# Optimization experiments

Hardware: AMD Instinct MI355X
Metric: run time of the kernel (lower is better)

## Reference

```python
import jax, jax.numpy as jnp
import numpy as np

N, D, E = 50000, 128, 100000
H1, H2, H3 = 8, 8, 4
NEG_SLOPE = 0.2  # PyG GATv2Conv default negative_slope


def _gatv2_layer(x, src, dst, Wl, Wr, att, b, heads):
    # GATv2Conv(in=D, out=D, heads=heads, concat=False), share_weights=False
    C = Wl.shape[1] // heads
    xl = (x @ Wl).reshape(-1, heads, C)  # source-side transform (x_j)
    xr = (x @ Wr).reshape(-1, heads, C)  # target-side transform (x_i)
    m = jax.nn.leaky_relu(xl[src] + xr[dst], NEG_SLOPE)      # [E,H,C]
    e = jnp.einsum('ehc,hc->eh', m, att)                      # [E,H]
    # segment softmax over incoming edges of each destination node
    emax = jax.ops.segment_max(e, dst, num_segments=N)        # [N,H]
    a = jnp.exp(e - emax[dst])
    denom = jax.ops.segment_sum(a, dst, num_segments=N)       # [N,H] (>0: self-loops)
    a = a / denom[dst]
    out = jax.ops.segment_sum(xl[src] * a[:, :, None], dst, num_segments=N)  # [N,H,C]
    return out.mean(axis=1) + b  # concat=False -> head mean, then bias


def setup_inputs() -> dict:
    key = jax.random.key(0)
    ks = jax.random.split(key, 16)
    x = jax.random.normal(ks[0], (N, D), dtype=jnp.float32)
    src = jax.random.randint(ks[1], (E,), 0, N)
    dst = jax.random.randint(ks[2], (E,), 0, N)
    src = jnp.where(src == dst, (src + 1) % N, src)  # no pre-existing self loops
    edge_index = jnp.stack([src, dst]).astype(jnp.int64)
    s = 1.0 / np.sqrt(D)
    def lin(k, h):
        return jax.random.uniform(k, (D, h * D), jnp.float32, -s, s)
    def attn(k, h):
        return jax.random.uniform(k, (h, D), jnp.float32, -s, s)
    return {
        'x': x, 'edge_index': edge_index,
        'W1l': lin(ks[3], H1), 'W1r': lin(ks[4], H1), 'att1': attn(ks[5], H1), 'b1': jnp.zeros((D,), jnp.float32),
        'W2l': lin(ks[6], H2), 'W2r': lin(ks[7], H2), 'att2': attn(ks[8], H2), 'b2': jnp.zeros((D,), jnp.float32),
        'W3l': lin(ks[9], H3), 'W3r': lin(ks[10], H3), 'att3': attn(ks[11], H3), 'b3': jnp.zeros((D,), jnp.float32),
    }


def reference(x, edge_index, W1l, W1r, att1, b1, W2l, W2r, att2, b2, W3l, W3r, att3, b3):
    # PyG GATv2Conv adds self loops by default
    loops = jnp.arange(N, dtype=edge_index.dtype)
    src = jnp.concatenate([edge_index[0], loops])
    dst = jnp.concatenate([edge_index[1], loops])
    h = x + _gatv2_layer(x, src, dst, W1l, W1r, att1, b1, H1)
    h = jax.nn.elu(h)  # dropout is identity in eval mode
    h = h + _gatv2_layer(h, src, dst, W2l, W2r, att2, b2, H2)
    h = jax.nn.elu(h)
    h = h + _gatv2_layer(h, src, dst, W3l, W3r, att3, b3, H3)
    return h
```

## Files before the change

kernel.cpp:

```cpp
#include <hip/hip_runtime.h>

#define NN 50000
#define DD 128
#define EE 100000
#define ET (EE + NN)

typedef __attribute__((ext_vector_type(4))) float f32x4;
typedef __attribute__((ext_vector_type(8))) short bf16x8;
typedef __attribute__((ext_vector_type(4))) unsigned short u16x4;
typedef __attribute__((ext_vector_type(4))) unsigned int u32x4;
typedef __attribute__((ext_vector_type(2))) unsigned int u32x2;

static __device__ __forceinline__ unsigned short f2bf(float f) {
  union { float f; unsigned int u; } v; v.f = f;
  unsigned int r = (v.u + 0x7FFFu + ((v.u >> 16) & 1u)) >> 16;
  return (unsigned short)r;
}
static __device__ __forceinline__ float bflo(unsigned int u) {
  union { unsigned int u; float f; } v; v.u = u << 16; return v.f;
}
static __device__ __forceinline__ float bfhi(unsigned int u) {
  union { unsigned int u; float f; } v; v.u = u & 0xffff0000u; return v.f;
}

template <int CTRL>
static __device__ __forceinline__ float dpp_add(float x) {
  int xi = __builtin_bit_cast(int, x);
  int yi = __builtin_amdgcn_update_dpp(xi, xi, CTRL, 0xF, 0xF, true);
  return x + __builtin_bit_cast(float, yi);
}
static __device__ __forceinline__ float row16_sum(float p) {
  p = dpp_add<0xB1>(p);
  p = dpp_add<0x4E>(p);
  p = dpp_add<0x141>(p);
  p = dpp_add<0x128>(p);
  return p;
}

__global__ __launch_bounds__(256) void k_prep(
    const float* __restrict__ x, const int* __restrict__ ei,
    const float* __restrict__ W1l, const float* __restrict__ W1r,
    const float* __restrict__ W2l, const float* __restrict__ W2r,
    const float* __restrict__ W3l, const float* __restrict__ W3r,
    const float* __restrict__ att1, const float* __restrict__ att2, const float* __restrict__ att3,
    unsigned short* __restrict__ wt1, unsigned short* __restrict__ wt2,
    unsigned short* __restrict__ wt3,
    float* __restrict__ as1, float* __restrict__ as2, float* __restrict__ as3,
    unsigned short* __restrict__ abf, int* __restrict__ counts) {
  const int i = blockIdx.x * 256 + threadIdx.x;
  const float LOG2E = 1.4426950408889634f;
  if (i < 262144) {
    int half = i >> 17, rem = i & 131071;
    int nn = rem >> 7, k = rem & 127;
    const float* W = half ? W1r : W1l;
    wt1[i] = f2bf(W[(size_t)k * 1024 + nn]);
  } else if (i < 524288) {
    int local = i - 262144;
    int half = local >> 17, rem = local & 131071;
    int nn = rem >> 7, k = rem & 127;
    const float* W = half ? W2r : W2l;
    wt2[local] = f2bf(W[(size_t)k * 1024 + nn]);
  } else if (i < 655360) {
    int local = i - 524288;
    int half = local >> 16, rem = local & 65535;
    int nn = rem >> 7, k = rem & 127;
    const float* W = half ? W3r : W3l;
    wt3[local] = f2bf(W[(size_t)k * 512 + nn]);
  } else if (i < 657920) {
    int local = i - 655360;
    if (local < 1024) as1[local] = att1[local] * LOG2E;
    else if (local < 2048) as2[local - 1024] = att2[local - 1024] * LOG2E;
    else as3[local - 2048] = att3[local - 2048] * LOG2E;
  } else if (i < 807920) {
    int e = i - 657920;
    int dst = (e < EE) ? ei[EE + e] : (e - EE);
    if (dst >= 0 && dst < NN) atomicAdd(&counts[dst], 1);
  } else if (i < 2407920) {
    int u = i - 807920;
    f32x4 v = *(const f32x4*)(x + (size_t)u * 4);
    u16x4 w;
    w.x = f2bf(v.x); w.y = f2bf(v.y); w.z = f2bf(v.z); w.w = f2bf(v.w);
    *(u16x4*)(abf + (size_t)u * 4) = w;
  }
}

__global__ __launch_bounds__(1024) void k_scan(const int* __restrict__ counts,
                                               int* __restrict__ offs,
                                               int* __restrict__ cursor) {
  __shared__ int wsum[16];
  __shared__ int wpre[16];
  __shared__ int wtot;
  const int tid = threadIdx.x;
  const int wv = tid >> 6, lane = tid & 63;
  int carry = 0;
  for (int base = 0; base < NN; base += 4096) {
    int i0 = base + tid * 4;
    int v[4];
#pragma unroll
    for (int q = 0; q < 4; ++q) { int i = i0 + q; v[q] = (i < NN) ? counts[i] : 0; }
    int s = v[0] + v[1] + v[2] + v[3];
    int sc = s;
#pragma unroll
    for (int m = 1; m < 64; m <<= 1) {
      int t = __shfl_up(sc, m, 64);
      if (lane >= m) sc += t;
    }
    if (lane == 63) wsum[wv] = sc;
    __syncthreads();
    if (tid < 16) {
      int t = wsum[tid];
      int scc = t;
#pragma unroll
      for (int m = 1; m < 16; m <<= 1) {
        int u = __shfl_up(scc, m, 64);
        if (tid >= m) scc += u;
      }
      wpre[tid] = scc - t;
      if (tid == 15) wtot = scc;
    }
    __syncthreads();
    int excl = carry + wpre[wv] + (sc - s);
#pragma unroll
    for (int q = 0; q < 4; ++q) {
      int i = i0 + q;
      if (i < NN) { offs[i] = excl; cursor[i] = excl; }
      excl += v[q];
    }
    carry += wtot;
    __syncthreads();
  }
  if (tid == 0) offs[NN] = carry;
}

__global__ void k_fill(const int* __restrict__ ei, int* __restrict__ cursor,
                       int* __restrict__ srcs) {
  int i = blockIdx.x * blockDim.x + threadIdx.x;
  if (i >= ET) return;
  int src, dst;
  if (i < EE) { src = ei[i]; dst = ei[EE + i]; }
  else { src = dst = i - EE; }
  if (dst < 0 || dst >= NN) return;
  if (src < 0 || src >= NN) src = dst;
  int pos = atomicAdd(&cursor[dst], 1);
  if (pos >= 0 && pos < ET) srcs[pos] = src;
}

__global__ __launch_bounds__(256) void gemm_bt(
    const unsigned short* __restrict__ A, const unsigned short* __restrict__ WT,
    unsigned short* __restrict__ Cl, unsigned short* __restrict__ Cr,
    int M, int Nout, int lgny) {
  const int f = blockIdx.x;
  const int c = f & ((1 << lgny) - 1);
  const int x = f >> lgny;
  const int z = c & 1, y = c >> 1;
  const int m0 = x * 128, n0 = y * 128;
  unsigned short* C = z ? Cr : Cl;
  const unsigned short* BT = WT + (size_t)z * Nout * DD;

  __shared__ unsigned short As[128 * 128];
  __shared__ unsigned short Bs[128 * 128];
  const int tid = threadIdx.x;
  const int wave = tid >> 6, lane = tid & 63;
  const int hi = lane >> 4, lr = lane & 15;

#pragma unroll
  for (int i = 0; i < 8; ++i) {
    int row = i * 16 + wave * 4 + hi;
    int c16 = lr ^ (row & 7);
    const unsigned short* ga = A + (size_t)(m0 + row) * DD + c16 * 8;
    __builtin_amdgcn_global_load_lds((const __attribute__((address_space(1))) void*)ga,
        (__attribute__((address_space(3))) void*)(As + i * 2048 + wave * 512), 16, 0, 0);
    const unsigned short* gb = BT + (size_t)(n0 + row) * DD + c16 * 8;
    __builtin_amdgcn_global_load_lds((const __attribute__((address_space(1))) void*)gb,
        (__attribute__((address_space(3))) void*)(Bs + i * 2048 + wave * 512), 16, 0, 0);
  }
  __syncthreads();

  const int wr = (wave >> 1) * 64, wc = (wave & 1) * 64;
  f32x4 acc[4][4];
#pragma unroll
  for (int i = 0; i < 4; ++i)
#pragma unroll
    for (int j = 0; j < 4; ++j) acc[i][j] = (f32x4){0.f, 0.f, 0.f, 0.f};

#pragma unroll
  for (int k0 = 0; k0 < 128; k0 += 32) {
    const int ck = (k0 >> 3) + hi;
    bf16x8 af[4], bfr[4];
#pragma unroll
    for (int mi = 0; mi < 4; ++mi) {
      int r = wr + mi * 16 + lr;
      af[mi] = *(const bf16x8*)&As[r * 128 + ((ck ^ (r & 7)) << 3)];
    }
#pragma unroll
    for (int ni = 0; ni < 4; ++ni) {
      int cc = wc + ni * 16 + lr;
      bfr[ni] = *(const bf16x8*)&Bs[cc * 128 + ((ck ^ (cc & 7)) << 3)];
    }
#pragma unroll
    for (int mi = 0; mi < 4; ++mi)
#pragma unroll
      for (int ni = 0; ni < 4; ++ni)
        acc[mi][ni] = __builtin_amdgcn_mfma_f32_16x16x32_bf16(af[mi], bfr[ni], acc[mi][ni], 0, 0, 0);
  }

#pragma unroll
  for (int mi = 0; mi < 4; ++mi) {
#pragma unroll
    for (int ni = 0; ni < 4; ++ni) {
      int col = n0 + wc + ni * 16 + lr;
#pragma unroll
      for (int j = 0; j < 4; ++j) {
        int row = m0 + wr + mi * 16 + (hi << 2) + j;
        if (row < M) C[(size_t)row * Nout + col] = f2bf(acc[mi][ni][j]);
      }
    }
  }
}

template <int H>
__global__ __launch_bounds__(256) void gat_agg5(
    const unsigned short* __restrict__ xl, const unsigned short* __restrict__ xr,
    const int* __restrict__ offs, const int* __restrict__ srcs,
    const float* __restrict__ att_s,
    const float* __restrict__ bias,
    const float* __restrict__ resid, float* __restrict__ out,
    unsigned short* __restrict__ hbf, int do_elu) {
  constexpr int HG = H / 2;
  constexpr int CPL = 2 * HG;
  constexpr int NW = HG;
  constexpr int LPH = 128 / CPL;
  constexpr int ROW = H * DD;
  constexpr int HALFROW = ROW / 2;
  const int wave = threadIdx.x >> 6, lane = threadIdx.x & 63;
  const int nsub = wave >> 1, g = wave & 1;
  const int n = blockIdx.x * 2 + nsub;
  if (n >= NN) return;
  const int cb = g * HALFROW + lane * CPL;

  float xrv[CPL], av[CPL];
  {
    const unsigned int* q = (const unsigned int*)(xr + (size_t)n * ROW + cb);
#pragma unroll
    for (int w = 0; w < NW; ++w) {
      unsigned int u = q[w];
      xrv[2 * w] = bflo(u);
      xrv[2 * w + 1] = bfhi(u);
    }
#pragma unroll
    for (int c = 0; c < CPL; ++c) av[c] = att_s[cb + c];
  }

  float acc[CPL];
#pragma unroll
  for (int c = 0; c < CPL; ++c) acc[c] = 0.f;
  float mx = -1e30f, dn = 0.f;

  const int e0 = offs[n], e1 = offs[n + 1];
  const unsigned short* xl_cb = xl + cb;
  for (int j = e0; j < e1; j += 4) {
    const int B = (e1 - j < 4) ? (e1 - j) : 4;
    unsigned int rows[4][NW];
#pragma unroll
    for (int b = 0; b < 4; ++b) {
      if (b < B) {
        int s = srcs[j + b];
        const unsigned int* qq = (const unsigned int*)(xl_cb + (size_t)s * ROW);
#pragma unroll
        for (int w = 0; w < NW; ++w) rows[b][w] = qq[w];
      }
    }
    float p[4];
#pragma unroll
    for (int b = 0; b < 4; ++b) {
      float pp = -1e30f;
      if (b < B) {
        pp = 0.f;
#pragma unroll
        for (int w = 0; w < NW; ++w) {
          float x0 = bflo(rows[b][w]), x1 = bfhi(rows[b][w]);
          float z0 = x0 + xrv[2 * w]; z0 = fmaxf(z0, 0.2f * z0);
          float z1 = x1 + xrv[2 * w + 1]; z1 = fmaxf(z1, 0.2f * z1);
          pp = fmaf(z0, av[2 * w], pp);
          pp = fmaf(z1, av[2 * w + 1], pp);
        }
        pp = row16_sum(pp);
        if constexpr (LPH == 32) pp += __shfl_xor(pp, 16, 64);
      }
      p[b] = pp;
    }
    float pm = fmaxf(fmaxf(p[0], p[1]), fmaxf(p[2], p[3]));
    if (__any(pm > mx + 11.5f)) {
      float mnew = fmaxf(mx, pm);
      float sc = __builtin_amdgcn_exp2f(mx - mnew);
      dn *= sc;
#pragma unroll
      for (int c = 0; c < CPL; ++c) acc[c] *= sc;
      mx = mnew;
    }
#pragma unroll
    for (int b = 0; b < 4; ++b) {
      if (b < B) {
        float wt = __builtin_amdgcn_exp2f(p[b] - mx);
        dn += wt;
#pragma unroll
        for (int w = 0; w < NW; ++w) {
          acc[2 * w] = fmaf(wt, bflo(rows[b][w]), acc[2 * w]);
          acc[2 * w + 1] = fmaf(wt, bfhi(rows[b][w]), acc[2 * w + 1]);
        }
      }
    }
  }

  float r[CPL];
  const float inv = (1.f / (float)H) / dn;
#pragma unroll
  for (int c = 0; c < CPL; ++c) r[c] = acc[c] * inv;
#pragma unroll
  for (int m = LPH; m < 64; m <<= 1)
#pragma unroll
    for (int c = 0; c < CPL; ++c) r[c] += __shfl_xor(r[c], m, 64);

  __shared__ float lds[2][DD];
  const int d0 = (lane * CPL) & 127;
  if (g == 1 && lane < LPH) {
#pragma unroll
    for (int c = 0; c < CPL; ++c) lds[nsub][d0 + c] = r[c];
  }
  __syncthreads();
  if (g == 0 && lane < LPH) {
    float o[CPL];
#pragma unroll
    for (int c = 0; c < CPL; ++c) {
      o[c] = r[c] + lds[nsub][d0 + c] + bias[d0 + c] + resid[(size_t)n * DD + d0 + c];
      if (do_elu && o[c] < 0.f)
        o[c] = __builtin_amdgcn_exp2f(o[c] * 1.4426950408889634f) - 1.f;
    }
#pragma unroll
    for (int c = 0; c < CPL; c += 4) {
      f32x4 v; v.x = o[c]; v.y = o[c + 1]; v.z = o[c + 2]; v.w = o[c + 3];
      *(f32x4*)(out + (size_t)n * DD + d0 + c) = v;
    }
    if (hbf) {
      unsigned int pk[CPL / 2];
#pragma unroll
      for (int q = 0; q < CPL / 2; ++q)
        pk[q] = (unsigned int)f2bf(o[2 * q]) | ((unsigned int)f2bf(o[2 * q + 1]) << 16);
      if constexpr (CPL == 8) {
        u32x4 v; v.x = pk[0]; v.y = pk[1]; v.z = pk[2]; v.w = pk[3];
        *(u32x4*)(hbf + (size_t)n * DD + d0) = v;
      } else {
        u32x2 v; v.x = pk[0]; v.y = pk[1];
        *(u32x2*)(hbf + (size_t)n * DD + d0) = v;
      }
    }
  }
}

extern "C" void kernel_launch(void* const* d_in, const int* in_sizes, int n_in,
                              void* d_out, int out_size, void* d_ws, size_t ws_size,
                              hipStream_t stream) {
  const float* x = (const float*)d_in[0];
  const int* ei = (const int*)d_in[1];
  const float* W1l = (const float*)d_in[2];
  const float* W1r = (const float*)d_in[3];
  const float* att1 = (const float*)d_in[4];
  const float* b1 = (const float*)d_in[5];
  const float* W2l = (const float*)d_in[6];
  const float* W2r = (const float*)d_in[7];
  const float* att2 = (const float*)d_in[8];
  const float* b2 = (const float*)d_in[9];
  const float* W3l = (const float*)d_in[10];
  const float* W3r = (const float*)d_in[11];
  const float* att3 = (const float*)d_in[12];
  const float* b3 = (const float*)d_in[13];
  float* out = (float*)d_out;

  char* p = (char*)d_ws;
  auto carve = [&](size_t bytes) {
    char* r = p;
    p += (bytes + 255) & ~(size_t)255;
    return r;
  };
  unsigned short* xl = (unsigned short*)carve((size_t)NN * 1024 * 2);
  unsigned short* xr = (unsigned short*)carve((size_t)NN * 1024 * 2);
  unsigned short* abf = (unsigned short*)carve((size_t)NN * DD * 2);
  unsigned short* wt1 = (unsigned short*)carve((size_t)2 * 1024 * DD * 2);
  unsigned short* wt2 = (unsigned short*)carve((size_t)2 * 1024 * DD * 2);
  unsigned short* wt3 = (unsigned short*)carve((size_t)2 * 512 * DD * 2);
  float* as1 = (float*)carve((size_t)8 * DD * 4);
  float* as2 = (float*)carve((size_t)8 * DD * 4);
  float* as3 = (float*)carve((size_t)4 * DD * 4);
  int* counts = (int*)carve((size_t)NN * 4);
  int* offs = (int*)carve(((size_t)NN + 1) * 4);
  int* cursor = (int*)carve((size_t)NN * 4);
  int* srcs = (int*)carve((size_t)ET * 4);
  size_t needed = (size_t)(p - (char*)d_ws);
  if (needed > ws_size) return;

  hipMemsetAsync(counts, 0, (size_t)NN * 4, stream);
  k_prep<<<9406, 256, 0, stream>>>(x, ei, W1l, W1r, W2l, W2r, W3l, W3r, att1, att2, att3,
                                   wt1, wt2, wt3, as1, as2, as3, abf, counts);
  k_scan<<<1, 1024, 0, stream>>>(counts, offs, cursor);
  k_fill<<<(ET + 255) / 256, 256, 0, stream>>>(ei, cursor, srcs);

  const int gx = (NN + 127) / 128;
  const int ga = (NN + 1) / 2;
  gemm_bt<<<gx * 16, 256, 0, stream>>>(abf, wt1, xl, xr, NN, 1024, 4);
  gat_agg5<8><<<ga, 256, 0, stream>>>(xl, xr, offs, srcs, as1, b1, x, out, abf, 1);
  gemm_bt<<<gx * 16, 256, 0, stream>>>(abf, wt2, xl, xr, NN, 1024, 4);
  gat_agg5<8><<<ga, 256, 0, stream>>>(xl, xr, offs, srcs, as2, b2, out, out, abf, 1);
  gemm_bt<<<gx * 8, 256, 0, stream>>>(abf, wt3, xl, xr, NN, 512, 3);
  gat_agg5<4><<<ga, 256, 0, stream>>>(xl, xr, offs, srcs, as3, b3, out, out, nullptr, 0);
}
```

Measured before the change: 472.2 us.

## Process four node pairs per block and batch eight edges per gather

The aggregation kernel now loops over four node pairs per block, so the launch is 6250 blocks instead of 25000. Attention weights and bias are loaded once per block rather than once per node, and a double-buffered LDS slot is used for the cross-wave reduction. The edge loop now gathers eight source rows per step instead of four, with the source indices prefetched first, to give more memory-level parallelism. The costs are higher register pressure from the 8-row buffer, which may lower occupancy, and fewer blocks to spread the irregular degree distribution across.

```diff
diff --git a/kernel.cpp b/kernel.cpp
--- a/kernel.cpp
+++ b/kernel.cpp
@@ -219,7 +219,7 @@
 }
 
 template <int H>
-__global__ __launch_bounds__(256) void gat_agg5(
+__global__ __launch_bounds__(256) void gat_agg6(
     const unsigned short* __restrict__ xl, const unsigned short* __restrict__ xr,
     const int* __restrict__ offs, const int* __restrict__ srcs,
     const float* __restrict__ att_s,
@@ -232,126 +232,139 @@
   constexpr int LPH = 128 / CPL;
   constexpr int ROW = H * DD;
   constexpr int HALFROW = ROW / 2;
+  constexpr int ITERS = 4;
   const int wave = threadIdx.x >> 6, lane = threadIdx.x & 63;
   const int nsub = wave >> 1, g = wave & 1;
-  const int n = blockIdx.x * 2 + nsub;
-  if (n >= NN) return;
   const int cb = g * HALFROW + lane * CPL;
-
-  float xrv[CPL], av[CPL];
-  {
-    const unsigned int* q = (const unsigned int*)(xr + (size_t)n * ROW + cb);
-#pragma unroll
-    for (int w = 0; w < NW; ++w) {
-      unsigned int u = q[w];
-      xrv[2 * w] = bflo(u);
-      xrv[2 * w + 1] = bfhi(u);
-    }
-#pragma unroll
-    for (int c = 0; c < CPL; ++c) av[c] = att_s[cb + c];
-  }
-
-  float acc[CPL];
-#pragma unroll
-  for (int c = 0; c < CPL; ++c) acc[c] = 0.f;
-  float mx = -1e30f, dn = 0.f;
-
-  const int e0 = offs[n], e1 = offs[n + 1];
+  const int d0 = (lane * CPL) & 127;
+
+  float av[CPL], bv[CPL];
+#pragma unroll
+  for (int c = 0; c < CPL; ++c) av[c] = att_s[cb + c];
+#pragma unroll
+  for (int c = 0; c < CPL; ++c) bv[c] = bias[d0 + c];
+
+  __shared__ float lds[2][2][DD];
   const unsigned short* xl_cb = xl + cb;
-  for (int j = e0; j < e1; j += 4) {
-    const int B = (e1 - j < 4) ? (e1 - j) : 4;
-    unsigned int rows[4][NW];
-#pragma unroll
-    for (int b = 0; b < 4; ++b) {
-      if (b < B) {
-        int s = srcs[j + b];
-        const unsigned int* qq = (const unsigned int*)(xl_cb + (size_t)s * ROW);
-#pragma unroll
-        for (int w = 0; w < NW; ++w) rows[b][w] = qq[w];
-      }
-    }
-    float p[4];
-#pragma unroll
-    for (int b = 0; b < 4; ++b) {
-      float pp = -1e30f;
-      if (b < B) {
-        pp = 0.f;
-#pragma unroll
-        for (int w = 0; w < NW; ++w) {
-          float x0 = bflo(rows[b][w]), x1 = bfhi(rows[b][w]);
-          float z0 = x0 + xrv[2 * w]; z0 = fmaxf(z0, 0.2f * z0);
-          float z1 = x1 + xrv[2 * w + 1]; z1 = fmaxf(z1, 0.2f * z1);
-          pp = fmaf(z0, av[2 * w], pp);
-          pp = fmaf(z1, av[2 * w + 1], pp);
+
+  for (int it = 0; it < ITERS; ++it) {
+    const int np = blockIdx.x * ITERS + it;
+    const int n = np * 2 + nsub;
+    const int e0 = offs[n], e1 = offs[n + 1];
+
+    float xrv[CPL];
+    {
+      const unsigned int* q = (const unsigned int*)(xr + (size_t)n * ROW + cb);
+#pragma unroll
+      for (int w = 0; w < NW; ++w) {
+        unsigned int u = q[w];
+        xrv[2 * w] = bflo(u);
+        xrv[2 * w + 1] = bfhi(u);
+      }
+    }
+    float acc[CPL];
+#pragma unroll
+    for (int c = 0; c < CPL; ++c) acc[c] = 0.f;
+    float mx = -1e30f, dn = 0.f;
+
+    for (int j = e0; j < e1; j += 8) {
+      const int B = (e1 - j < 8) ? (e1 - j) : 8;
+      int sv[8];
+#pragma unroll
+      for (int b = 0; b < 8; ++b) sv[b] = (b < B) ? srcs[j + b] : 0;
+      unsigned int rows[8][NW];
+#pragma unroll
+      for (int b = 0; b < 8; ++b) {
+        if (b < B) {
+          const unsigned int* qq = (const unsigned int*)(xl_cb + (size_t)sv[b] * ROW);
+#pragma unroll
+          for (int w = 0; w < NW; ++w) rows[b][w] = qq[w];
         }
-        pp = row16_sum(pp);
-        if constexpr (LPH == 32) pp += __shfl_xor(pp, 16, 64);
-      }
-      p[b] = pp;
-    }
-    float pm = fmaxf(fmaxf(p[0], p[1]), fmaxf(p[2], p[3]));
-    if (__any(pm > mx + 11.5f)) {
-      float mnew = fmaxf(mx, pm);
-      float sc = __builtin_amdgcn_exp2f(mx - mnew);
-      dn *= sc;
-#pragma unroll
-      for (int c = 0; c < CPL; ++c) acc[c] *= sc;
-      mx = mnew;
-    }
-#pragma unroll
-    for (int b = 0; b < 4; ++b) {
-      if (b < B) {
-        float wt = __builtin_amdgcn_exp2f(p[b] - mx);
-        dn += wt;
-#pragma unroll
-        for (int w = 0; w < NW; ++w) {
-          acc[2 * w] = fmaf(wt, bflo(rows[b][w]), acc[2 * w]);
-          acc[2 * w + 1] = fmaf(wt, bfhi(rows[b][w]), acc[2 * w + 1]);
+      }
+      float p[8];
+#pragma unroll
+      for (int b = 0; b < 8; ++b) {
+        float pp = -1e30f;
+        if (b < B) {
+          pp = 0.f;
+#pragma unroll
+          for (int w = 0; w < NW; ++w) {
+            float x0 = bflo(rows[b][w]), x1 = bfhi(rows[b][w]);
+            float z0 = x0 + xrv[2 * w]; z0 = fmaxf(z0, 0.2f * z0);
+            float z1 = x1 + xrv[2 * w + 1]; z1 = fmaxf(z1, 0.2f * z1);
+            pp = fmaf(z0, av[2 * w], pp);
+            pp = fmaf(z1, av[2 * w + 1], pp);
+          }
+          pp = row16_sum(pp);
+          if constexpr (LPH == 32) pp += __shfl_xor(pp, 16, 64);
         }
-      }
-    }
-  }
-
-  float r[CPL];
-  const float inv = (1.f / (float)H) / dn;
-#pragma unroll
-  for (int c = 0; c < CPL; ++c) r[c] = acc[c] * inv;
-#pragma unroll
-  for (int m = LPH; m < 64; m <<= 1)
-#pragma unroll
-    for (int c = 0; c < CPL; ++c) r[c] += __shfl_xor(r[c], m, 64);
-
-  __shared__ float lds[2][DD];
-  const int d0 = (lane * CPL) & 127;
-  if (g == 1 && lane < LPH) {
-#pragma unroll
-    for (int c = 0; c < CPL; ++c) lds[nsub][d0 + c] = r[c];
-  }
-  __syncthreads();
-  if (g == 0 && lane < LPH) {
-    float o[CPL];
-#pragma unroll
-    for (int c = 0; c < CPL; ++c) {
-      o[c] = r[c] + lds[nsub][d0 + c] + bias[d0 + c] + resid[(size_t)n * DD + d0 + c];
-      if (do_elu && o[c] < 0.f)
-        o[c] = __builtin_amdgcn_exp2f(o[c] * 1.4426950408889634f) - 1.f;
-    }
-#pragma unroll
-    for (int c = 0; c < CPL; c += 4) {
-      f32x4 v; v.x = o[c]; v.y = o[c + 1]; v.z = o[c + 2]; v.w = o[c + 3];
-      *(f32x4*)(out + (size_t)n * DD + d0 + c) = v;
-    }
-    if (hbf) {
-      unsigned int pk[CPL / 2];
-#pragma unroll
-      for (int q = 0; q < CPL / 2; ++q)
-        pk[q] = (unsigned int)f2bf(o[2 * q]) | ((unsigned int)f2bf(o[2 * q + 1]) << 16);
-      if constexpr (CPL == 8) {
-        u32x4 v; v.x = pk[0]; v.y = pk[1]; v.z = pk[2]; v.w = pk[3];
-        *(u32x4*)(hbf + (size_t)n * DD + d0) = v;
-      } else {
-        u32x2 v; v.x = pk[0]; v.y = pk[1];
-        *(u32x2*)(hbf + (size_t)n * DD + d0) = v;
+        p[b] = pp;
+      }
+      float pm = p[0];
+#pragma unroll
+      for (int b = 1; b < 8; ++b) pm = fmaxf(pm, p[b]);
+      if (__any(pm > mx + 11.5f)) {
+        float mnew = fmaxf(mx, pm);
+        float sc = __builtin_amdgcn_exp2f(mx - mnew);
+        dn *= sc;
+#pragma unroll
+        for (int c = 0; c < CPL; ++c) acc[c] *= sc;
+        mx = mnew;
+      }
+#pragma unroll
+      for (int b = 0; b < 8; ++b) {
+        if (b < B) {
+          float wt = __builtin_amdgcn_exp2f(p[b] - mx);
+          dn += wt;
+#pragma unroll
+          for (int w = 0; w < NW; ++w) {
+            acc[2 * w] = fmaf(wt, bflo(rows[b][w]), acc[2 * w]);
+            acc[2 * w + 1] = fmaf(wt, bfhi(rows[b][w]), acc[2 * w + 1]);
+          }
+        }
+      }
+    }
+
+    float r[CPL];
+    const float inv = (1.f / (float)H) / dn;
+#pragma unroll
+    for (int c = 0; c < CPL; ++c) r[c] = acc[c] * inv;
+#pragma unroll
+    for (int m = LPH; m < 64; m <<= 1)
+#pragma unroll
+      for (int c = 0; c < CPL; ++c) r[c] += __shfl_xor(r[c], m, 64);
+
+    const int par = it & 1;
+    if (g == 1 && lane < LPH) {
+#pragma unroll
+      for (int c = 0; c < CPL; ++c) lds[par][nsub][d0 + c] = r[c];
+    }
+    __syncthreads();
+    if (g == 0 && lane < LPH) {
+      float o[CPL];
+#pragma unroll
+      for (int c = 0; c < CPL; ++c) {
+        o[c] = r[c] + lds[par][nsub][d0 + c] + bv[c] + resid[(size_t)n * DD + d0 + c];
+        if (do_elu && o[c] < 0.f)
+          o[c] = __builtin_amdgcn_exp2f(o[c] * 1.4426950408889634f) - 1.f;
+      }
+#pragma unroll
+      for (int c = 0; c < CPL; c += 4) {
+        f32x4 v; v.x = o[c]; v.y = o[c + 1]; v.z = o[c + 2]; v.w = o[c + 3];
+        *(f32x4*)(out + (size_t)n * DD + d0 + c) = v;
+      }
+      if (hbf) {
+        unsigned int pk[CPL / 2];
+#pragma unroll
+        for (int q = 0; q < CPL / 2; ++q)
+          pk[q] = (unsigned int)f2bf(o[2 * q]) | ((unsigned int)f2bf(o[2 * q + 1]) << 16);
+        if constexpr (CPL == 8) {
+          u32x4 v; v.x = pk[0]; v.y = pk[1]; v.z = pk[2]; v.w = pk[3];
+          *(u32x4*)(hbf + (size_t)n * DD + d0) = v;
+        } else {
+          u32x2 v; v.x = pk[0]; v.y = pk[1];
+          *(u32x2*)(hbf + (size_t)n * DD + d0) = v;
+        }
       }
     }
   }
@@ -405,11 +418,11 @@
   k_fill<<<(ET + 255) / 256, 256, 0, stream>>>(ei, cursor, srcs);
 
   const int gx = (NN + 127) / 128;
-  const int ga = (NN + 1) / 2;
+  const int ga = NN / 8;
   gemm_bt<<<gx * 16, 256, 0, stream>>>(abf, wt1, xl, xr, NN, 1024, 4);
-  gat_agg5<8><<<ga, 256, 0, stream>>>(xl, xr, offs, srcs, as1, b1, x, out, abf, 1);
+  gat_agg6<8><<<ga, 256, 0, stream>>>(xl, xr, offs, srcs, as1, b1, x, out, abf, 1);
   gemm_bt<<<gx * 16, 256, 0, stream>>>(abf, wt2, xl, xr, NN, 1024, 4);
-  gat_agg5<8><<<ga, 256, 0, stream>>>(xl, xr, offs, srcs, as2, b2, out, out, abf, 1);
+  gat_agg6<8><<<ga, 256, 0, stream>>>(xl, xr, offs, srcs, as2, b2, out, out, abf, 1);
   gemm_bt<<<gx * 8, 256, 0, stream>>>(abf, wt3, xl, xr, NN, 512, 3);
-  gat_agg5<4><<<ga, 256, 0, stream>>>(xl, xr, offs, srcs, as3, b3, out, out, nullptr, 0);
-}
+  gat_agg6<4><<<ga, 256, 0, stream>>>(xl, xr, offs, srcs, as3, b3, out, out, nullptr, 0);
+}
```

After: 570.2 us. +20.8%, slower.

## Make GAT aggregation persistent and carry residual through bf16 buffer only

Applied to the files above, without the earlier changes.

The aggregation kernel becomes a persistent grid-stride loop over node pairs with a fixed grid of 2048 blocks, double-buffering the shared-memory exchange between the two half-row waves. Layers 1 and 2 no longer write the fp32 hidden state; layers 2 and 3 read their residual from the bf16 activation buffer instead of an fp32 copy. The aim is to cut global memory traffic and block launch overhead in the aggregation passes. In exchange the residual path is rounded to bf16, which adds a small accuracy loss, and the fixed grid may balance work across nodes with uneven degree less well.

```diff
diff --git a/kernel.cpp b/kernel.cpp
--- a/kernel.cpp
+++ b/kernel.cpp
@@ -219,13 +219,16 @@
 }
 
 template <int H>
-__global__ __launch_bounds__(256) void gat_agg5(
+__global__ __launch_bounds__(256) void gat_agg7(
     const unsigned short* __restrict__ xl, const unsigned short* __restrict__ xr,
     const int* __restrict__ offs, const int* __restrict__ srcs,
     const float* __restrict__ att_s,
     const float* __restrict__ bias,
-    const float* __restrict__ resid, float* __restrict__ out,
-    unsigned short* __restrict__ hbf, int do_elu) {
+    const float* __restrict__ residf,
+    const unsigned short* __restrict__ residb,
+    float* __restrict__ outf,
+    unsigned short* __restrict__ hbfw,
+    int do_elu) {
   constexpr int HG = H / 2;
   constexpr int CPL = 2 * HG;
   constexpr int NW = HG;
@@ -234,126 +237,150 @@
   constexpr int HALFROW = ROW / 2;
   const int wave = threadIdx.x >> 6, lane = threadIdx.x & 63;
   const int nsub = wave >> 1, g = wave & 1;
-  const int n = blockIdx.x * 2 + nsub;
-  if (n >= NN) return;
   const int cb = g * HALFROW + lane * CPL;
-
-  float xrv[CPL], av[CPL];
-  {
-    const unsigned int* q = (const unsigned int*)(xr + (size_t)n * ROW + cb);
-#pragma unroll
-    for (int w = 0; w < NW; ++w) {
-      unsigned int u = q[w];
-      xrv[2 * w] = bflo(u);
-      xrv[2 * w + 1] = bfhi(u);
-    }
-#pragma unroll
-    for (int c = 0; c < CPL; ++c) av[c] = att_s[cb + c];
-  }
-
-  float acc[CPL];
-#pragma unroll
-  for (int c = 0; c < CPL; ++c) acc[c] = 0.f;
-  float mx = -1e30f, dn = 0.f;
-
-  const int e0 = offs[n], e1 = offs[n + 1];
+  const int d0 = (lane * CPL) & 127;
+
+  float av[CPL];
+#pragma unroll
+  for (int c = 0; c < CPL; ++c) av[c] = att_s[cb + c];
+
+  __shared__ float lds[2][2][DD];
   const unsigned short* xl_cb = xl + cb;
-  for (int j = e0; j < e1; j += 4) {
-    const int B = (e1 - j < 4) ? (e1 - j) : 4;
-    unsigned int rows[4][NW];
-#pragma unroll
-    for (int b = 0; b < 4; ++b) {
-      if (b < B) {
-        int s = srcs[j + b];
-        const unsigned int* qq = (const unsigned int*)(xl_cb + (size_t)s * ROW);
-#pragma unroll
-        for (int w = 0; w < NW; ++w) rows[b][w] = qq[w];
-      }
-    }
-    float p[4];
-#pragma unroll
-    for (int b = 0; b < 4; ++b) {
-      float pp = -1e30f;
-      if (b < B) {
-        pp = 0.f;
-#pragma unroll
-        for (int w = 0; w < NW; ++w) {
-          float x0 = bflo(rows[b][w]), x1 = bfhi(rows[b][w]);
-          float z0 = x0 + xrv[2 * w]; z0 = fmaxf(z0, 0.2f * z0);
-          float z1 = x1 + xrv[2 * w + 1]; z1 = fmaxf(z1, 0.2f * z1);
-          pp = fmaf(z0, av[2 * w], pp);
-          pp = fmaf(z1, av[2 * w + 1], pp);
-        }
-        pp = row16_sum(pp);
-        if constexpr (LPH == 32) pp += __shfl_xor(pp, 16, 64);
-      }
-      p[b] = pp;
-    }
-    float pm = fmaxf(fmaxf(p[0], p[1]), fmaxf(p[2], p[3]));
-    if (__any(pm > mx + 11.5f)) {
-      float mnew = fmaxf(mx, pm);
-      float sc = __builtin_amdgcn_exp2f(mx - mnew);
-      dn *= sc;
-#pragma unroll
-      for (int c = 0; c < CPL; ++c) acc[c] *= sc;
-      mx = mnew;
-    }
-#pragma unroll
-    for (int b = 0; b < 4; ++b) {
-      if (b < B) {
-        float wt = __builtin_amdgcn_exp2f(p[b] - mx);
-        dn += wt;
-#pragma unroll
-        for (int w = 0; w < NW; ++w) {
-          acc[2 * w] = fmaf(wt, bflo(rows[b][w]), acc[2 * w]);
-          acc[2 * w + 1] = fmaf(wt, bfhi(rows[b][w]), acc[2 * w + 1]);
-        }
-      }
-    }
-  }
-
-  float r[CPL];
-  const float inv = (1.f / (float)H) / dn;
-#pragma unroll
-  for (int c = 0; c < CPL; ++c) r[c] = acc[c] * inv;
-#pragma unroll
-  for (int m = LPH; m < 64; m <<= 1)
-#pragma unroll
-    for (int c = 0; c < CPL; ++c) r[c] += __shfl_xor(r[c], m, 64);
-
-  __shared__ float lds[2][DD];
-  const int d0 = (lane * CPL) & 127;
-  if (g == 1 && lane < LPH) {
-#pragma unroll
-    for (int c = 0; c < CPL; ++c) lds[nsub][d0 + c] = r[c];
-  }
-  __syncthreads();
-  if (g == 0 && lane < LPH) {
-    float o[CPL];
-#pragma unroll
-    for (int c = 0; c < CPL; ++c) {
-      o[c] = r[c] + lds[nsub][d0 + c] + bias[d0 + c] + resid[(size_t)n * DD + d0 + c];
-      if (do_elu && o[c] < 0.f)
-        o[c] = __builtin_amdgcn_exp2f(o[c] * 1.4426950408889634f) - 1.f;
-    }
-#pragma unroll
-    for (int c = 0; c < CPL; c += 4) {
-      f32x4 v; v.x = o[c]; v.y = o[c + 1]; v.z = o[c + 2]; v.w = o[c + 3];
-      *(f32x4*)(out + (size_t)n * DD + d0 + c) = v;
-    }
-    if (hbf) {
-      unsigned int pk[CPL / 2];
-#pragma unroll
-      for (int q = 0; q < CPL / 2; ++q)
-        pk[q] = (unsigned int)f2bf(o[2 * q]) | ((unsigned int)f2bf(o[2 * q + 1]) << 16);
-      if constexpr (CPL == 8) {
-        u32x4 v; v.x = pk[0]; v.y = pk[1]; v.z = pk[2]; v.w = pk[3];
-        *(u32x4*)(hbf + (size_t)n * DD + d0) = v;
+  const int stride = gridDim.x * 2;
+  int par = 0;
+
+  for (int n = blockIdx.x * 2 + nsub; n < NN; n += stride) {
+    const int e0 = offs[n], e1 = offs[n + 1];
+
+    float xrv[CPL];
+    {
+      const unsigned int* q = (const unsigned int*)(xr + (size_t)n * ROW + cb);
+#pragma unroll
+      for (int w = 0; w < NW; ++w) {
+        unsigned int u = q[w];
+        xrv[2 * w] = bflo(u);
+        xrv[2 * w + 1] = bfhi(u);
+      }
+    }
+    float acc[CPL];
+#pragma unroll
+    for (int c = 0; c < CPL; ++c) acc[c] = 0.f;
+    float mx = -1e30f, dn = 0.f;
+
+    for (int j = e0; j < e1; j += 4) {
+      const int B = (e1 - j < 4) ? (e1 - j) : 4;
+      unsigned int rows[4][NW];
+#pragma unroll
+      for (int b = 0; b < 4; ++b) {
+        if (b < B) {
+          int s = srcs[j + b];
+          const unsigned int* qq = (const unsigned int*)(xl_cb + (size_t)s * ROW);
+#pragma unroll
+          for (int w = 0; w < NW; ++w) rows[b][w] = qq[w];
+        }
+      }
+      float p[4];
+#pragma unroll
+      for (int b = 0; b < 4; ++b) {
+        float pp = -1e30f;
+        if (b < B) {
+          pp = 0.f;
+#pragma unroll
+          for (int w = 0; w < NW; ++w) {
+            float x0 = bflo(rows[b][w]), x1 = bfhi(rows[b][w]);
+            float z0 = x0 + xrv[2 * w]; z0 = fmaxf(z0, 0.2f * z0);
+            float z1 = x1 + xrv[2 * w + 1]; z1 = fmaxf(z1, 0.2f * z1);
+            pp = fmaf(z0, av[2 * w], pp);
+            pp = fmaf(z1, av[2 * w + 1], pp);
+          }
+          pp = row16_sum(pp);
+          if constexpr (LPH == 32) pp += __shfl_xor(pp, 16, 64);
+        }
+        p[b] = pp;
+      }
+      float pm = fmaxf(fmaxf(p[0], p[1]), fmaxf(p[2], p[3]));
+      if (__any(pm > mx + 11.5f)) {
+        float mnew = fmaxf(mx, pm);
+        float sc = __builtin_amdgcn_exp2f(mx - mnew);
+        dn *= sc;
+#pragma unroll
+        for (int c = 0; c < CPL; ++c) acc[c] *= sc;
+        mx = mnew;
+      }
+#pragma unroll
+      for (int b = 0; b < 4; ++b) {
+        if (b < B) {
+          float wt = __builtin_amdgcn_exp2f(p[b] - mx);
+          dn += wt;
+#pragma unroll
+          for (int w = 0; w < NW; ++w) {
+            acc[2 * w] = fmaf(wt, bflo(rows[b][w]), acc[2 * w]);
+            acc[2 * w + 1] = fmaf(wt, bfhi(rows[b][w]), acc[2 * w + 1]);
+          }
+        }
+      }
+    }
+
+    float r[CPL];
+    const float inv = (1.f / (float)H) / dn;
+#pragma unroll
+    for (int c = 0; c < CPL; ++c) r[c] = acc[c] * inv;
+#pragma unroll
+    for (int m = LPH; m < 64; m <<= 1)
+#pragma unroll
+      for (int c = 0; c < CPL; ++c) r[c] += __shfl_xor(r[c], m, 64);
+
+    if (g == 1 && lane < LPH) {
+#pragma unroll
+      for (int c = 0; c < CPL; ++c) lds[par][nsub][d0 + c] = r[c];
+    }
+    __syncthreads();
+    if (g == 0 && lane < LPH) {
+      float rv[CPL];
+      if (residf) {
+#pragma unroll
+        for (int c = 0; c < CPL; c += 4) {
+          f32x4 v = *(const f32x4*)(residf + (size_t)n * DD + d0 + c);
+          rv[c] = v.x; rv[c + 1] = v.y; rv[c + 2] = v.z; rv[c + 3] = v.w;
+        }
       } else {
-        u32x2 v; v.x = pk[0]; v.y = pk[1];
-        *(u32x2*)(hbf + (size_t)n * DD + d0) = v;
-      }
-    }
+        const unsigned int* q = (const unsigned int*)(residb + (size_t)n * DD + d0);
+#pragma unroll
+        for (int w = 0; w < CPL / 2; ++w) {
+          unsigned int u = q[w];
+          rv[2 * w] = bflo(u);
+          rv[2 * w + 1] = bfhi(u);
+        }
+      }
+      float o[CPL];
+#pragma unroll
+      for (int c = 0; c < CPL; ++c) {
+        o[c] = r[c] + lds[par][nsub][d0 + c] + bias[d0 + c] + rv[c];
+        if (do_elu && o[c] < 0.f)
+          o[c] = __builtin_amdgcn_exp2f(o[c] * 1.4426950408889634f) - 1.f;
+      }
+      if (outf) {
+#pragma unroll
+        for (int c = 0; c < CPL; c += 4) {
+          f32x4 v; v.x = o[c]; v.y = o[c + 1]; v.z = o[c + 2]; v.w = o[c + 3];
+          *(f32x4*)(outf + (size_t)n * DD + d0 + c) = v;
+        }
+      }
+      if (hbfw) {
+        unsigned int pk[CPL / 2];
+#pragma unroll
+        for (int q = 0; q < CPL / 2; ++q)
+          pk[q] = (unsigned int)f2bf(o[2 * q]) | ((unsigned int)f2bf(o[2 * q + 1]) << 16);
+        if constexpr (CPL == 8) {
+          u32x4 v; v.x = pk[0]; v.y = pk[1]; v.z = pk[2]; v.w = pk[3];
+          *(u32x4*)(hbfw + (size_t)n * DD + d0) = v;
+        } else {
+          u32x2 v; v.x = pk[0]; v.y = pk[1];
+          *(u32x2*)(hbfw + (size_t)n * DD + d0) = v;
+        }
+      }
+    }
+    par ^= 1;
   }
 }
 
@@ -405,11 +432,14 @@
   k_fill<<<(ET + 255) / 256, 256, 0, stream>>>(ei, cursor, srcs);
 
   const int gx = (NN + 127) / 128;
-  const int ga = (NN + 1) / 2;
+  const int ga = 2048;
   gemm_bt<<<gx * 16, 256, 0, stream>>>(abf, wt1, xl, xr, NN, 1024, 4);
-  gat_agg5<8><<<ga, 256, 0, stream>>>(xl, xr, offs, srcs, as1, b1, x, out, abf, 1);
+  gat_agg7<8><<<ga, 256, 0, stream>>>(xl, xr, offs, srcs, as1, b1, x, nullptr,
+                                      nullptr, abf, 1);
   gemm_bt<<<gx * 16, 256, 0, stream>>>(abf, wt2, xl, xr, NN, 1024, 4);
-  gat_agg5<8><<<ga, 256, 0, stream>>>(xl, xr, offs, srcs, as2, b2, out, out, abf, 1);
+  gat_agg7<8><<<ga, 256, 0, stream>>>(xl, xr, offs, srcs, as2, b2, nullptr, abf,
+                                      nullptr, abf, 1);
   gemm_bt<<<gx * 8, 256, 0, stream>>>(abf, wt3, xl, xr, NN, 512, 3);
-  gat_agg5<4><<<ga, 256, 0, stream>>>(xl, xr, offs, srcs, as3, b3, out, out, nullptr, 0);
-}
+  gat_agg7<4><<<ga, 256, 0, stream>>>(xl, xr, offs, srcs, as3, b3, nullptr, abf,
+                                      out, nullptr, 0);
+}
```

After: 534.7 us. 1.13x slower.
